# Kernel tuning notes

Hardware: AMD Instinct MI355X
Metric: run time of the kernel (lower is better)

Reference implementation:

```python
import jax, jax.numpy as jnp
import numpy as np

B, S, D = 8, 2048, 1024

def setup_inputs() -> dict:
    key = jax.random.key(0)
    k1, k2 = jax.random.split(key)
    x = jax.random.normal(k1, (B, S, D), dtype=jnp.float32)
    # nn.Linear(dim, dim, bias=False) weight: [out, in]
    W = jax.random.normal(k2, (D, D), dtype=jnp.float32) * (1.0 / np.sqrt(D))
    return {"x": x, "W": W}

def reference(x, W):
    d = x.shape[-1]
    scale = 1.0 / jnp.sqrt(jnp.float32(d))
    # scores: [B, S, S]
    scores = jnp.einsum('bqd,bkd->bqk', x, x) * scale
    S_len = x.shape[-2]
    causal = jnp.tril(jnp.ones((S_len, S_len), dtype=bool))  # keep lower triangle incl. diag
    scores = jnp.where(causal[None, :, :], scores, -jnp.inf)
    attn_w = jax.nn.softmax(scores, axis=-1)
    attn = jnp.einsum('bqk,bkd->bqd', attn_w, x)
    # nn.Linear: y = attn @ W.T
    return jnp.einsum('bqd,ed->bqe', attn, W)
```

## Files before the change

kernel.cpp:

```cpp
#include <hip/hip_runtime.h>

typedef __attribute__((ext_vector_type(8))) __bf16 bf16x8;
typedef __attribute__((ext_vector_type(4))) float floatx4;

static __device__ __forceinline__ floatx4 mfma16(bf16x8 a, bf16x8 b, floatx4 c) {
  return __builtin_amdgcn_mfma_f32_16x16x32_bf16(a, b, c, 0, 0, 0);
}

static __device__ __forceinline__ unsigned short f2b_bits(float f) {
  __bf16 h = (__bf16)f;
  return __builtin_bit_cast(unsigned short, h);
}

static __device__ __forceinline__ void stage16(const void* g, void* l) {
  __builtin_amdgcn_global_load_lds(
      (__attribute__((address_space(1))) void*)(unsigned long long)g,
      (__attribute__((address_space(3))) void*)(unsigned int)(unsigned long long)l,
      16, 0, 0);
}

#define VM6B() asm volatile("s_waitcnt vmcnt(6)\n\ts_barrier" ::: "memory")
#define VM3B() asm volatile("s_waitcnt vmcnt(3)\n\ts_barrier" ::: "memory")
#define VM0B() asm volatile("s_waitcnt vmcnt(0)\n\ts_barrier" ::: "memory")
#define BAR()  asm volatile("s_barrier" ::: "memory")


__global__ void cast_kernel(const float4* __restrict__ x, const float4* __restrict__ w,
                            ushort4* __restrict__ xb, ushort4* __restrict__ wb,
                            float* __restrict__ lsum) {
  int i = blockIdx.x * 256 + threadIdx.x;
  if (i < 2097152) {
    const int c = i >> 6, s = i & 63;
    const int R = (c >> 5) * 16 + (s & 15);
    const int kg = (c & 31) * 4 + (s >> 4);
    float4 v0 = x[R * 256 + kg * 2];
    float4 v1 = x[R * 256 + kg * 2 + 1];
    ushort4 o0, o1;
    o0.x = f2b_bits(v0.x); o0.y = f2b_bits(v0.y); o0.z = f2b_bits(v0.z); o0.w = f2b_bits(v0.w);
    o1.x = f2b_bits(v1.x); o1.y = f2b_bits(v1.y); o1.z = f2b_bits(v1.z); o1.w = f2b_bits(v1.w);
    xb[i * 2] = o0; xb[i * 2 + 1] = o1;
  } else if (i < 2228224) {
    const int i2 = i - 2097152;
    const int c = i2 >> 6, s = i2 & 63;
    const int R = (c >> 5) * 16 + (s & 15);
    const int kg = (c & 31) * 4 + (s >> 4);
    float4 v0 = w[R * 256 + kg * 2];
    float4 v1 = w[R * 256 + kg * 2 + 1];
    ushort4 o0, o1;
    o0.x = f2b_bits(v0.x); o0.y = f2b_bits(v0.y); o0.z = f2b_bits(v0.z); o0.w = f2b_bits(v0.w);
    o1.x = f2b_bits(v1.x); o1.y = f2b_bits(v1.y); o1.z = f2b_bits(v1.z); o1.w = f2b_bits(v1.w);
    wb[i2 * 2] = o0; wb[i2 * 2 + 1] = o1;
  } else {
    const int j = i - 2228224;
    if (j < 16384) lsum[j] = 0.0f;
  }
}


__global__ __launch_bounds__(512, 2) void zq_fused(const unsigned short* __restrict__ xb,
                                                   const unsigned short* __restrict__ wb,
                                                   unsigned short* __restrict__ zT,
                                                   unsigned short* __restrict__ P,
                                                   float* __restrict__ lsum) {
  extern __shared__ bf16x8 lds[];
  bf16x8* ldsA = lds;
  bf16x8* ldsB = lds + 1536;
  const int tid = threadIdx.x, wid = tid >> 6, lane = tid & 63;
  const int wr = wid >> 2, wc = wid & 3, lr = lane & 15, lq = lane >> 4;
  const int g = blockIdx.x;
  const bool is_qk = (g >= 512);

  const unsigned short* gA;
  const unsigned short* gB0;
  const unsigned short* gB1;
  int b, mt, ntl, rt, ct;
  if (!is_qk) {
    b = g & 7;
    const int gg = g >> 3;
    mt = gg >> 2; ntl = gg & 3;
    gA = xb + ((size_t)b * 4096 + (mt * 8 + wid) * 32) * 512 + lane * 8;
    gB0 = wb + (size_t)((ntl * 16 + wid) * 32) * 512 + lane * 8;
    gB1 = wb + (size_t)((ntl * 16 + wid + 8) * 32) * 512 + lane * 8;
  } else {
    const int h = g - 512;
    b = h & 7;
    const int idx = h >> 3;
    int m = (int)((sqrtf(4.0f * idx + 1.0f) - 1.0f) * 0.5f);
    while ((m + 1) * (m + 2) <= idx) ++m;
    while (m * (m + 1) > idx) --m;
    const int rem = idx - m * (m + 1);
    rt = 2 * m + (rem > m);
    ct = rem - (rem > m ? (m + 1) : 0);
    gA = xb + ((size_t)b * 4096 + (rt * 8 + wid) * 32) * 512 + lane * 8;
    gB0 = xb + ((size_t)b * 4096 + (ct * 16 + wid) * 32) * 512 + lane * 8;
    gB1 = xb + ((size_t)b * 4096 + (ct * 16 + wid + 8) * 32) * 512 + lane * 8;
  }

  floatx4 acc[4][4] = {};

#pragma unroll
  for (int t = 0; t < 2; ++t) {
    stage16(gA + t * 512, &ldsA[t * 512 + wid * 64]);
    stage16(gB0 + t * 512, &ldsB[t * 1024 + wid * 64]);
    stage16(gB1 + t * 512, &ldsB[t * 1024 + (wid + 8) * 64]);
  }

#pragma unroll
  for (int kt = 0; kt < 32; ++kt) {
    const int cb = kt % 3;
    if (kt + 2 < 32) {
      const int sb = (kt + 2) % 3;
      stage16(gA + (kt + 2) * 512, &ldsA[sb * 512 + wid * 64]);
      stage16(gB0 + (kt + 2) * 512, &ldsB[sb * 1024 + wid * 64]);
      stage16(gB1 + (kt + 2) * 512, &ldsB[sb * 1024 + (wid + 8) * 64]);
      VM6B();
    } else if (kt + 1 < 32) {
      VM3B();
    } else {
      VM0B();
    }
    bf16x8 a_[4], b_[4];
#pragma unroll
    for (int i = 0; i < 4; ++i) a_[i] = ldsA[cb * 512 + (wr * 4 + i) * 64 + lane];
#pragma unroll
    for (int j = 0; j < 4; ++j) b_[j] = ldsB[cb * 1024 + (wc * 4 + j) * 64 + lane];
#pragma unroll
    for (int i = 0; i < 4; ++i)
#pragma unroll
      for (int j = 0; j < 4; ++j) acc[i][j] = mfma16(a_[i], b_[j], acc[i][j]);
    BAR();
  }

  if (!is_qk) {
#pragma unroll
    for (int i = 0; i < 4; ++i) {
      const int s0 = mt * 128 + wr * 64 + i * 16 + lq * 4;
      const int s5 = s0 >> 5, s3 = (s0 >> 3) & 3, s7 = s0 & 7;
#pragma unroll
      for (int j = 0; j < 4; ++j) {
        const int e4 = ntl * 16 + wc * 4 + j;
        ushort4 o;
        o.x = f2b_bits(acc[i][j][0]); o.y = f2b_bits(acc[i][j][1]);
        o.z = f2b_bits(acc[i][j][2]); o.w = f2b_bits(acc[i][j][3]);
        *(ushort4*)(zT + ((size_t)b * 4096 + e4 * 64 + s5) * 512 + s3 * 128 + lr * 8 + s7) = o;
      }
    }
  } else {
    const int col128 = 2 * ct + (wc >> 1);
    if (col128 <= rt) {
      const bool diag = (col128 == rt);
      unsigned short* Pt =
          P + ((size_t)b * 136 + (size_t)(rt * (rt + 1) / 2 + col128)) * 16384;
      float* lsb = lsum + b * 2048 + rt * 128;
#pragma unroll
      for (int i = 0; i < 4; ++i) {
        const int row_l = wr * 64 + i * 16 + lq * 4;
        floatx4 rs = {0.0f, 0.0f, 0.0f, 0.0f};
#pragma unroll
        for (int j = 0; j < 4; ++j) {
          const int incol = (wc & 1) * 64 + j * 16 + lr;
          const int cbase = ((wr * 4 + i) * 4 + (wc & 1) * 2 + (j >> 1)) * 512 +
                            ((j * 2 + (lr >> 3)) & 3) * 128 + (lr & 7);
#pragma unroll
          for (int v = 0; v < 4; ++v) {
            float p = __expf(acc[i][j][v] * 0.03125f - 44.0f);
            if (diag && incol > row_l + v) p = 0.0f;
            Pt[cbase + (lq * 4 + v) * 8] = f2b_bits(p);
            rs[v] += p;
          }
        }
#pragma unroll
        for (int v = 0; v < 4; ++v) {
          float s = rs[v];
          s += __shfl_xor(s, 1);
          s += __shfl_xor(s, 2);
          s += __shfl_xor(s, 4);
          s += __shfl_xor(s, 8);
          if (lr == 0) atomicAdd(&lsb[row_l + v], s);
        }
      }
    }
  }
}

__global__ __launch_bounds__(512, 2) void pv_out(const unsigned short* __restrict__ P,
                                                 const unsigned short* __restrict__ zT,
                                                 const float* __restrict__ lsum,
                                                 float* __restrict__ out) {
  extern __shared__ bf16x8 lds[];
  bf16x8* ldsA = lds;
  bf16x8* ldsB = lds + 1536;
  const int tid = threadIdx.x, wid = tid >> 6, lane = tid & 63;
  const int wr = wid >> 2, wc = wid & 3, lr = lane & 15, lq = lane >> 4;
  const int g = blockIdx.x, b = g & 7, gg = g >> 3;
  const int rt = 15 - (gg >> 2), ntl = gg & 3;
  const int NKT = (rt + 1) * 4;

  const unsigned short* pA =
      P + ((size_t)b * 136 + (size_t)(rt * (rt + 1) / 2)) * 16384 + (size_t)wid * 2048 + lane * 8;
  const unsigned short* gB0 = zT + ((size_t)b * 4096 + (ntl * 16 + wid) * 64) * 512 + lane * 8;
  const unsigned short* gB1 =
      zT + ((size_t)b * 4096 + (ntl * 16 + wid + 8) * 64) * 512 + lane * 8;
  floatx4 acc[4][4] = {};

#pragma unroll
  for (int t = 0; t < 2; ++t) {
    stage16(pA + (t >> 2) * 16384 + (t & 3) * 512, &ldsA[t * 512 + wid * 64]);
    stage16(gB0 + t * 512, &ldsB[t * 1024 + wid * 64]);
    stage16(gB1 + t * 512, &ldsB[t * 1024 + (wid + 8) * 64]);
  }

  int cb = 0, sb = 2;
  for (int kt = 0; kt < NKT; ++kt) {
    if (kt + 2 < NKT) {
      const int k2 = kt + 2;
      stage16(pA + (k2 >> 2) * 16384 + (k2 & 3) * 512, &ldsA[sb * 512 + wid * 64]);
      stage16(gB0 + k2 * 512, &ldsB[sb * 1024 + wid * 64]);
      stage16(gB1 + k2 * 512, &ldsB[sb * 1024 + (wid + 8) * 64]);
      VM6B();
    } else if (kt + 1 < NKT) {
      VM3B();
    } else {
      VM0B();
    }
    bf16x8 a_[4], b_[4];
#pragma unroll
    for (int i = 0; i < 4; ++i) a_[i] = ldsA[cb * 512 + (wr * 4 + i) * 64 + lane];
#pragma unroll
    for (int j = 0; j < 4; ++j) b_[j] = ldsB[cb * 1024 + (wc * 4 + j) * 64 + lane];
#pragma unroll
    for (int i = 0; i < 4; ++i)
#pragma unroll
      for (int j = 0; j < 4; ++j) acc[i][j] = mfma16(a_[i], b_[j], acc[i][j]);
    BAR();
    cb = (cb == 2) ? 0 : cb + 1;
    sb = (sb == 2) ? 0 : sb + 1;
  }

  const float* lsb = lsum + b * 2048 + rt * 128;
  float* outb = out + (size_t)b * 2097152;
#pragma unroll
  for (int i = 0; i < 4; ++i) {
    const int row_l = wr * 64 + i * 16 + lq * 4;
    floatx4 linv;
#pragma unroll
    for (int v = 0; v < 4; ++v) linv[v] = 1.0f / lsb[row_l + v];
#pragma unroll
    for (int j = 0; j < 4; ++j) {
      const int col = ntl * 256 + wc * 64 + j * 16 + lr;
#pragma unroll
      for (int v = 0; v < 4; ++v)
        __builtin_nontemporal_store(acc[i][j][v] * linv[v],
                                    &outb[(size_t)(rt * 128 + row_l + v) * 1024 + col]);
    }
  }
}

extern "C" void kernel_launch(void* const* d_in, const int* in_sizes, int n_in,
                              void* d_out, int out_size, void* d_ws, size_t ws_size,
                              hipStream_t stream) {
  const float* x = (const float*)d_in[0];
  const float* W = (const float*)d_in[1];
  float* out = (float*)d_out;
  char* ws = (char*)d_ws;
  unsigned short* xb = (unsigned short*)ws;
  unsigned short* zT = (unsigned short*)(ws + 33554432ull);
  unsigned short* P  = (unsigned short*)(ws + 67108864ull);
  unsigned short* wb = (unsigned short*)(ws + 67108864ull + 35651584ull + 65536ull);
  float* lsum = (float*)(ws + 67108864ull + 35651584ull);

  static bool attr_done = false;
  if (!attr_done) {
    (void)hipFuncSetAttribute(reinterpret_cast<const void*>(zq_fused),
                              hipFuncAttributeMaxDynamicSharedMemorySize, 73728);
    (void)hipFuncSetAttribute(reinterpret_cast<const void*>(pv_out),
                              hipFuncAttributeMaxDynamicSharedMemorySize, 73728);
    attr_done = true;
  }

  cast_kernel<<<8768, 256, 0, stream>>>((const float4*)x, (const float4*)W,
                                        (ushort4*)xb, (ushort4*)wb, lsum);
  zq_fused<<<1088, 512, 73728, stream>>>(xb, wb, zT, P, lsum);
  pv_out<<<512, 512, 73728, stream>>>(P, zT, lsum, out);
}
```

Baseline: 229.9 us.

## Stage cast tiles through swizzled LDS and reorder pv_out row-tile scheduling

The cast kernel now gives each block a 16-row tile. Each thread reads coalesced float4 values from global memory and writes bf16 into XOR-swizzled shared memory, then emits the MFMA-friendly layout as 16-byte stores. Previously the scattered tile layout came straight from strided global reads. This targets poor load coalescing in the conversion pass and cuts the grid from 8768 small blocks to 1092. Separately, pv_out maps blocks to row tiles so the second half runs ascending instead of descending, changing how long and short causal blocks are interleaved for load balance.

```diff
diff --git a/kernel.cpp b/kernel.cpp
--- a/kernel.cpp
+++ b/kernel.cpp
@@ -25,34 +25,37 @@
 #define BAR()  asm volatile("s_barrier" ::: "memory")
 
 
-__global__ void cast_kernel(const float4* __restrict__ x, const float4* __restrict__ w,
-                            ushort4* __restrict__ xb, ushort4* __restrict__ wb,
-                            float* __restrict__ lsum) {
-  int i = blockIdx.x * 256 + threadIdx.x;
-  if (i < 2097152) {
-    const int c = i >> 6, s = i & 63;
-    const int R = (c >> 5) * 16 + (s & 15);
-    const int kg = (c & 31) * 4 + (s >> 4);
-    float4 v0 = x[R * 256 + kg * 2];
-    float4 v1 = x[R * 256 + kg * 2 + 1];
-    ushort4 o0, o1;
-    o0.x = f2b_bits(v0.x); o0.y = f2b_bits(v0.y); o0.z = f2b_bits(v0.z); o0.w = f2b_bits(v0.w);
-    o1.x = f2b_bits(v1.x); o1.y = f2b_bits(v1.y); o1.z = f2b_bits(v1.z); o1.w = f2b_bits(v1.w);
-    xb[i * 2] = o0; xb[i * 2 + 1] = o1;
-  } else if (i < 2228224) {
-    const int i2 = i - 2097152;
-    const int c = i2 >> 6, s = i2 & 63;
-    const int R = (c >> 5) * 16 + (s & 15);
-    const int kg = (c & 31) * 4 + (s >> 4);
-    float4 v0 = w[R * 256 + kg * 2];
-    float4 v1 = w[R * 256 + kg * 2 + 1];
-    ushort4 o0, o1;
-    o0.x = f2b_bits(v0.x); o0.y = f2b_bits(v0.y); o0.z = f2b_bits(v0.z); o0.w = f2b_bits(v0.w);
-    o1.x = f2b_bits(v1.x); o1.y = f2b_bits(v1.y); o1.z = f2b_bits(v1.z); o1.w = f2b_bits(v1.w);
-    wb[i2 * 2] = o0; wb[i2 * 2 + 1] = o1;
+__global__ __launch_bounds__(256) void cast_kernel(const float4* __restrict__ x,
+                                                   const float4* __restrict__ w,
+                                                   uint4* __restrict__ xb,
+                                                   uint4* __restrict__ wb,
+                                                   float4* __restrict__ lsum) {
+  __shared__ unsigned char sl[32768];
+  const int st = blockIdx.x, tid = threadIdx.x;
+  if (st < 1088) {
+    const float4* src = (st < 1024) ? x + (size_t)st * 4096 : w + (size_t)(st - 1024) * 4096;
+    uint4* dst = (st < 1024) ? xb + (size_t)st * 2048 : wb + (size_t)(st - 1024) * 2048;
+#pragma unroll
+    for (int it = 0; it < 16; ++it) {
+      const int row = it, c4 = (it * 256 + tid) & 255;
+      float4 v = src[row * 256 + c4];
+      ushort4 o;
+      o.x = f2b_bits(v.x); o.y = f2b_bits(v.y); o.z = f2b_bits(v.z); o.w = f2b_bits(v.w);
+      *(ushort4*)(sl + row * 2048 + ((c4 * 8) ^ ((row & 7) << 4))) = o;
+    }
+    __syncthreads();
+#pragma unroll
+    for (int it = 0; it < 8; ++it) {
+      const int o = it * 4096 + tid * 16;
+      const int c = o >> 10, l = (o >> 4) & 63;
+      const int row = l & 15, kg = l >> 4;
+      uint4 v = *(const uint4*)(sl + row * 2048 + ((c * 64 + kg * 16) ^ ((row & 7) << 4)));
+      dst[o >> 4] = v;
+    }
   } else {
-    const int j = i - 2228224;
-    if (j < 16384) lsum[j] = 0.0f;
+    const float4 z = {0.0f, 0.0f, 0.0f, 0.0f};
+#pragma unroll
+    for (int it = 0; it < 4; ++it) lsum[(st - 1088) * 1024 + it * 256 + tid] = z;
   }
 }
 
@@ -193,7 +196,9 @@
   const int tid = threadIdx.x, wid = tid >> 6, lane = tid & 63;
   const int wr = wid >> 2, wc = wid & 3, lr = lane & 15, lq = lane >> 4;
   const int g = blockIdx.x, b = g & 7, gg = g >> 3;
-  const int rt = 15 - (gg >> 2), ntl = gg & 3;
+  const int q = gg >> 2;
+  const int rt = (gg < 32) ? 15 - q : q - 8;
+  const int ntl = gg & 3;
   const int NKT = (rt + 1) * 4;
 
   const unsigned short* pA =
@@ -278,8 +283,8 @@
     attr_done = true;
   }
 
-  cast_kernel<<<8768, 256, 0, stream>>>((const float4*)x, (const float4*)W,
-                                        (ushort4*)xb, (ushort4*)wb, lsum);
+  cast_kernel<<<1092, 256, 0, stream>>>((const float4*)x, (const float4*)W,
+                                        (uint4*)xb, (uint4*)wb, (float4*)lsum);
   zq_fused<<<1088, 512, 73728, stream>>>(xb, wb, zT, P, lsum);
   pv_out<<<512, 512, 73728, stream>>>(P, zT, lsum, out);
 }
```

After: 229.5 us. No clear change (-0.2%).
